# Optimization experiments

Measured on AMD Instinct MI355X. Metric: run time of the kernel, lower is better.

The kernel has to match this reference:

```python
import jax, jax.numpy as jnp
import numpy as np

B, T, F = 64, 512, 512      # batch, timesteps, raw feature dim
D_IN = 1024                 # input_layer units
H = 1024                    # hidden_units
D_OUT = 128                 # output_size


def setup_inputs() -> dict:
    key = jax.random.key(0)
    ks = jax.random.split(key, 10)
    def glorot(k, shape):
        lim = np.sqrt(6.0 / (shape[0] + shape[1])).astype(np.float32)
        return jax.random.uniform(k, shape, jnp.float32, -lim, lim)
    return {
        "x": jax.random.normal(ks[0], (B, T, F), jnp.float32),
        # input Dense (tanh)
        "Wi": glorot(ks[1], (F, D_IN)),
        "bi": jnp.zeros((D_IN,), jnp.float32),
        # LSTM layer 0: kernel, recurrent kernel, bias (init ones, gate order i,f,c,o)
        "W0": glorot(ks[2], (D_IN, 4 * H)),
        "U0": glorot(ks[3], (H, 4 * H)),
        "b0": jnp.ones((4 * H,), jnp.float32),
        # LSTM layer 1
        "W1": glorot(ks[4], (H, 4 * H)),
        "U1": glorot(ks[5], (H, 4 * H)),
        "b1": jnp.ones((4 * H,), jnp.float32),
        # output Dense (tanh)
        "Wo": glorot(ks[6], (H, D_OUT)),
        "bo": jnp.zeros((D_OUT,), jnp.float32),
    }


def _lstm_cell(x, h, c, W, U, b):
    # Keras LSTMCell gate order: i, f, c(candidate), o
    z = x @ W + h @ U + b                      # [B, 4H]
    zi, zf, zc, zo = jnp.split(z, 4, axis=-1)
    i = jax.nn.sigmoid(zi)
    f = jax.nn.sigmoid(zf)
    c_new = f * c + i * jnp.tanh(zc)
    h_new = jax.nn.sigmoid(zo) * jnp.tanh(c_new)
    return h_new, c_new


def reference(x, Wi, bi, W0, U0, b0, W1, U1, b1, Wo, bo):
    b = x.shape[0]
    h = W0.shape[1] // 4
    zeros = jnp.zeros((b, h), x.dtype)
    init = (zeros, zeros, zeros, zeros)  # h0, c0, h1, c1

    def step(carry, xt):
        h0, c0, h1, c1 = carry
        xin = jnp.tanh(xt @ Wi + bi)                    # input Dense
        h0, c0 = _lstm_cell(xin, h0, c0, W0, U0, b0)
        h1, c1 = _lstm_cell(h0, h1, c1, W1, U1, b1)
        return (h0, c0, h1, c1), None

    (h0, c0, h1, c1), _ = jax.lax.scan(step, init, jnp.swapaxes(x, 0, 1))
    return jnp.tanh(h1 @ Wo + bo)  # [B, D_OUT]
```

## Files before the change

### kernel.cpp

```cpp
#include <hip/hip_runtime.h>
#include <math.h>

#define BB 64
#define TT 512
#define FF 512
#define DIN 1024
#define HH 1024
#define G4 4096
#define DOUT 128

typedef _Float16 f16;
typedef _Float16 f16x4 __attribute__((ext_vector_type(4)));
typedef _Float16 f16x8 __attribute__((ext_vector_type(8)));
typedef float f32x4 __attribute__((ext_vector_type(4)));

__device__ __forceinline__ size_t afrag_off(int m, int k) {
    return (size_t)(((k >> 5) * 4 + (m >> 4)) * 512 + (((((k >> 3) & 3) << 4) | (m & 15)) * 8) + (k & 7));
}

__device__ __forceinline__ void store_b128_sc1(void* p, f32x4 v) {
    asm volatile("global_store_dwordx4 %0, %1, off sc1" :: "v"(p), "v"(v) : "memory");
}

__global__ __launch_bounds__(64) void k_pack(
    const float* __restrict__ W, const float* __restrict__ U, f16* __restrict__ out)
{
    const int kstep = blockIdx.x, cg = blockIdx.y, l = threadIdx.x;
    const int n = l & 15, q = l >> 4;
    const int stdcol = (n & 3) * HH + cg * 4 + (n >> 2);
    f16x8 v;
#pragma unroll
    for (int e = 0; e < 8; ++e) {
        int k = kstep * 32 + q * 8 + e;
        float s = (k < DIN) ? W[(size_t)k * G4 + stdcol] : U[(size_t)(k - DIN) * G4 + stdcol];
        v[e] = (f16)s;
    }
    *(f16x8*)(out + ((size_t)(cg * 64 + kstep) * 64 + l) * 8) = v;
}

__global__ __launch_bounds__(64) void k_pack_wi(
    const float* __restrict__ Wi, f16* __restrict__ out)
{
    const int kstep = blockIdx.x;
    const int nt    = blockIdx.y;
    const int l = threadIdx.x;
    const int n = nt * 16 + (l & 15), q = l >> 4;
    f16x8 v;
#pragma unroll
    for (int e = 0; e < 8; ++e)
        v[e] = (f16)Wi[(size_t)(kstep * 32 + q * 8 + e) * DIN + n];
    *(f16x8*)(out + ((size_t)(nt * 16 + kstep) * 64 + l) * 8) = v;
}

__global__ __launch_bounds__(256) void k_dense_in2(
    const float* __restrict__ x, const f16* __restrict__ pWi,
    const float* __restrict__ bi, f16* __restrict__ XinF)
{
    extern __shared__ f16 xs[];
    const int t = blockIdx.x;
    const int tid = threadIdx.x;

#pragma unroll
    for (int it = 0; it < 32; ++it) {
        int idx = tid + it * 256;
        int r = idx >> 7, c4 = idx & 127;
        float4 v = *(const float4*)(x + ((size_t)r * TT + t) * FF + c4 * 4);
        f16x4 hv = {(f16)v.x, (f16)v.y, (f16)v.z, (f16)v.w};
        *(f16x4*)(xs + (size_t)r * 520 + c4 * 4) = hv;
    }
    __syncthreads();

    const int w = tid >> 6, lane = tid & 63;
    const int col = lane & 15, rq = lane >> 4;
#pragma unroll 1
    for (int g = 0; g < 4; ++g) {
        f32x4 acc[4][4];
#pragma unroll
        for (int a = 0; a < 4; ++a)
#pragma unroll
            for (int b = 0; b < 4; ++b) acc[a][b] = (f32x4){0.f, 0.f, 0.f, 0.f};
#pragma unroll 2
        for (int ks2 = 0; ks2 < 16; ++ks2) {
            f16x8 bf[4];
#pragma unroll
            for (int nn = 0; nn < 4; ++nn)
                bf[nn] = *(const f16x8*)(pWi + ((size_t)((w * 16 + g * 4 + nn) * 16 + ks2) * 64 + lane) * 8);
#pragma unroll
            for (int mt = 0; mt < 4; ++mt) {
                f16x8 af = *(const f16x8*)(xs + (size_t)(mt * 16 + col) * 520 + ks2 * 32 + rq * 8);
#pragma unroll
                for (int nn = 0; nn < 4; ++nn)
                    acc[mt][nn] = __builtin_amdgcn_mfma_f32_16x16x32_f16(af, bf[nn], acc[mt][nn], 0, 0, 0);
            }
        }
#pragma unroll
        for (int nn = 0; nn < 4; ++nn) {
            const int j = (w * 16 + g * 4 + nn) * 16 + col;
            const float bb = bi[j];
#pragma unroll
            for (int mt = 0; mt < 4; ++mt)
#pragma unroll
                for (int r = 0; r < 4; ++r)
                    XinF[(size_t)t * (BB * DIN) + afrag_off(mt * 16 + rq * 4 + r, j)]
                        = (f16)tanhf(acc[mt][nn][r] + bb);
        }
    }
}

__global__ __launch_bounds__(512, 2) void k_persist(
    const f16* __restrict__ XinF,
    f16* __restrict__ h0b_, f16* __restrict__ h1b_,
    const f16* __restrict__ pW0, const f16* __restrict__ pW1,
    const float* __restrict__ b0, const float* __restrict__ b1,
    unsigned* __restrict__ flags)
{
    extern __shared__ char smem[];
    f16*   bsh = (f16*)smem;
    float* red = (float*)(smem + 131072);

    const int lay = blockIdx.x & 1;
    const int cgb = blockIdx.x >> 1;
    const int tid = threadIdx.x;
    const int wv = tid >> 6, lane = tid & 63;
    const int kq = wv >> 1, mh = wv & 1;

    unsigned* fl   = flags + (lay ? 1024 : 0);
    unsigned* goO  = flags + 2048 + (lay ? 32 : 0);
    unsigned* go0p = flags + 2048;
    const bool isAgg = (cgb == 0);

    {
        const f16x8* s8 = (const f16x8*)((lay ? pW1 : pW0) + (size_t)(cgb * 2) * 64 * 512);
        f16x8* d8 = (f16x8*)bsh;
#pragma unroll
        for (int it = 0; it < 16; ++it) d8[tid + it * 512] = s8[tid + it * 512];
    }

    const float* bias = lay ? b1 : b0;
    const int erow = tid & 63, ejl = (tid >> 6) & 3;
    const int emt = erow >> 4, esub = erow & 15;
    const int eslq = (esub >> 2) << 4, ereg = esub & 3;
    float bz[2][4];
    float creg[2] = {0.f, 0.f};
    if (tid < 256) {
#pragma unroll
        for (int n = 0; n < 2; ++n) {
            const int jg = (cgb * 2 + n) * 4 + ejl;
#pragma unroll
            for (int g = 0; g < 4; ++g) bz[n][g] = bias[g * HH + jg];
        }
    }

    const size_t HBUF = (size_t)BB * DIN;
    const f16* bq = bsh + (size_t)(kq * 16 * 64 + lane) * 8;
    __syncthreads();

    for (int p = 0; p <= TT; ++p) {
        if (lay == 0 && p == TT) break;
        const bool active = lay ? (p >= 1) : true;

        if (active) {
            const f16* Abase;
            if (lay == 0) Abase = (kq < 2) ? (XinF + (size_t)p * HBUF) : (h0b_ + (size_t)p * HBUF);
            else          Abase = (kq < 2) ? (h0b_ + (size_t)p * HBUF) : (h1b_ + (size_t)(p - 1) * HBUF);
            f16* hw = lay ? (h1b_ + (size_t)p * HBUF) : (h0b_ + (size_t)(p + 1) * HBUF);
            const f16* Ap = Abase + (size_t)(((kq & 1) * 64 + mh * 2) * 512) + (size_t)lane * 8;

            f16x8 a0v[16], a1v[16];
            const bool pre = (lay == 0) && (kq < 2);
            if (pre) {
#pragma unroll
                for (int ii = 0; ii < 16; ++ii) {
                    a0v[ii] = *(const f16x8*)(Ap + (size_t)(ii * 4) * 512);
                    a1v[ii] = *(const f16x8*)(Ap + (size_t)(ii * 4 + 1) * 512);
                }
            }

            if (lay == 0) {
                if (p > 0) {
                    if (tid == 0)
                        while (__hip_atomic_load(go0p, __ATOMIC_RELAXED, __HIP_MEMORY_SCOPE_AGENT) < (unsigned)p)
                            __builtin_amdgcn_s_sleep(1);
                    __syncthreads();
                }
            } else {
                if (tid == 0) {
                    while (__hip_atomic_load(go0p, __ATOMIC_RELAXED, __HIP_MEMORY_SCOPE_AGENT) < (unsigned)p)
                        __builtin_amdgcn_s_sleep(1);
                    while (__hip_atomic_load(goO, __ATOMIC_RELAXED, __HIP_MEMORY_SCOPE_AGENT) < (unsigned)p)
                        __builtin_amdgcn_s_sleep(1);
                }
                __syncthreads();
            }

            if (!pre) {
#pragma unroll
                for (int ii = 0; ii < 16; ++ii) {
                    a0v[ii] = *(const f16x8*)(Ap + (size_t)(ii * 4) * 512);
                    a1v[ii] = *(const f16x8*)(Ap + (size_t)(ii * 4 + 1) * 512);
                }
            }

            f32x4 acc00 = {0.f,0.f,0.f,0.f}, acc01 = {0.f,0.f,0.f,0.f};
            f32x4 acc10 = {0.f,0.f,0.f,0.f}, acc11 = {0.f,0.f,0.f,0.f};
#pragma unroll
            for (int ii = 0; ii < 16; ++ii) {
                f16x8 bb0 = *(const f16x8*)(bq + (size_t)ii * 512);
                f16x8 bb1 = *(const f16x8*)(bq + 32768 + (size_t)ii * 512);
                acc00 = __builtin_amdgcn_mfma_f32_16x16x32_f16(a0v[ii], bb0, acc00, 0, 0, 0);
                acc01 = __builtin_amdgcn_mfma_f32_16x16x32_f16(a0v[ii], bb1, acc01, 0, 0, 0);
                acc10 = __builtin_amdgcn_mfma_f32_16x16x32_f16(a1v[ii], bb0, acc10, 0, 0, 0);
                acc11 = __builtin_amdgcn_mfma_f32_16x16x32_f16(a1v[ii], bb1, acc11, 0, 0, 0);
            }

            f16 hvv[2];
#pragma unroll
            for (int n = 0; n < 2; ++n) {
                f32x4 t0 = n ? acc01 : acc00;
                f32x4 t1 = n ? acc11 : acc10;
                *(f32x4*)(red + (size_t)(kq * 4 + mh * 2)     * 260 + lane * 4) = t0;
                *(f32x4*)(red + (size_t)(kq * 4 + mh * 2 + 1) * 260 + lane * 4) = t1;
                __syncthreads();
                if (tid < 256) {
                    float z[4];
#pragma unroll
                    for (int g = 0; g < 4; ++g) {
                        const int sl = eslq | (ejl * 4 + g);
                        float s = 0.f;
#pragma unroll
                        for (int k2 = 0; k2 < 4; ++k2)
                            s += red[(size_t)(k2 * 4 + emt) * 260 + sl * 4 + ereg];
                        z[g] = s + bz[n][g];
                    }
                    const float ig = 1.f / (1.f + expf(-z[0]));
                    const float fg = 1.f / (1.f + expf(-z[1]));
                    const float cc = tanhf(z[2]);
                    const float og = 1.f / (1.f + expf(-z[3]));
                    const float cn = fg * creg[n] + ig * cc;
                    creg[n] = cn;
                    hvv[n] = (f16)(og * tanhf(cn));
                }
                __syncthreads();
            }

            f16* hrow = (f16*)red;
            if (tid < 256) {
                hrow[erow * 8 + ejl]     = hvv[0];
                hrow[erow * 8 + 4 + ejl] = hvv[1];
            }
            __syncthreads();
            if (tid < 64) {
                f32x4 v = *(f32x4*)(hrow + tid * 8);
                store_b128_sc1(hw + afrag_off(tid, cgb * 8), v);
            }
        }

        asm volatile("s_waitcnt vmcnt(0)" ::: "memory");
        __syncthreads();
        const unsigned tgt = (unsigned)(p + 1);
        if (tid == 0)
            __hip_atomic_store(&fl[cgb], tgt, __ATOMIC_RELAXED, __HIP_MEMORY_SCOPE_AGENT);
        if (isAgg) {
            if (tid < 64) {
                for (;;) {
                    bool ok = (__hip_atomic_load(&fl[lane], __ATOMIC_RELAXED, __HIP_MEMORY_SCOPE_AGENT) >= tgt)
                           && (__hip_atomic_load(&fl[lane + 64], __ATOMIC_RELAXED, __HIP_MEMORY_SCOPE_AGENT) >= tgt);
                    if (__all(ok)) break;
                    __builtin_amdgcn_s_sleep(1);
                }
                if (tid == 0)
                    __hip_atomic_store(goO, tgt, __ATOMIC_RELAXED, __HIP_MEMORY_SCOPE_AGENT);
            }
        }
    }
}

__global__ __launch_bounds__(128) void k_out(
    const f16* __restrict__ h1f, const float* __restrict__ Wo,
    const float* __restrict__ bo, float* __restrict__ out)
{
    __shared__ float hs[HH];
    const int b = blockIdx.x;
    for (int i = threadIdx.x; i < HH; i += 128) hs[i] = (float)h1f[afrag_off(b, i)];
    __syncthreads();
    const int o = threadIdx.x;
    float acc = 0.f;
    for (int k = 0; k < HH; ++k) acc += hs[k] * Wo[k * DOUT + o];
    out[b * DOUT + o] = tanhf(acc + bo[o]);
}

extern "C" void kernel_launch(void* const* d_in, const int* in_sizes, int n_in,
                              void* d_out, int out_size, void* d_ws, size_t ws_size,
                              hipStream_t stream)
{
    const float* x  = (const float*)d_in[0];
    const float* Wi = (const float*)d_in[1];
    const float* bi = (const float*)d_in[2];
    const float* W0 = (const float*)d_in[3];
    const float* U0 = (const float*)d_in[4];
    const float* b0 = (const float*)d_in[5];
    const float* W1 = (const float*)d_in[6];
    const float* U1 = (const float*)d_in[7];
    const float* b1 = (const float*)d_in[8];
    const float* Wo = (const float*)d_in[9];
    const float* bo = (const float*)d_in[10];
    float* out = (float*)d_out;

    f16* ws16 = (f16*)d_ws;
    const size_t HBUF = (size_t)BB * DIN;
    f16* XinF = ws16;
    f16* pW0  = XinF + (size_t)TT * HBUF;
    f16* pW1  = pW0 + (size_t)2048 * G4;
    f16* pWi  = pW1 + (size_t)2048 * G4;
    f16* h0   = pWi + (size_t)FF * DIN;
    f16* h1   = h0 + (size_t)513 * HBUF;
    unsigned* flags = (unsigned*)(h1 + (size_t)513 * HBUF);

    hipMemsetAsync(h0, 0, HBUF * sizeof(f16), stream);
    hipMemsetAsync(h1, 0, HBUF * sizeof(f16), stream);
    hipMemsetAsync(flags, 0, 16384, stream);

    k_pack<<<dim3(64, 256), 64, 0, stream>>>(W0, U0, pW0);
    k_pack<<<dim3(64, 256), 64, 0, stream>>>(W1, U1, pW1);
    k_pack_wi<<<dim3(16, 64), 64, 0, stream>>>(Wi, pWi);

    hipFuncSetAttribute((const void*)k_dense_in2,
                        hipFuncAttributeMaxDynamicSharedMemorySize, 66560);
    k_dense_in2<<<TT, 256, 66560, stream>>>(x, pWi, bi, XinF);

    {
        const int smem_bytes = 131072 + 16640;
        hipFuncSetAttribute((const void*)k_persist,
                            hipFuncAttributeMaxDynamicSharedMemorySize, smem_bytes);
        const f16* XinF_c = XinF;
        const f16* pW0_c = pW0;
        const f16* pW1_c = pW1;
        f16 *h0_v = h0, *h1_v = h1;
        const float *b0_v = b0, *b1_v = b1;
        unsigned* flags_v = flags;
        void* kargs[] = {
            (void*)&XinF_c,
            (void*)&h0_v, (void*)&h1_v,
            (void*)&pW0_c, (void*)&pW1_c,
            (void*)&b0_v, (void*)&b1_v,
            (void*)&flags_v
        };
        hipLaunchCooperativeKernel((void*)k_persist, dim3(256), dim3(512),
                                   kargs, smem_bytes, stream);
    }

    k_out<<<BB, 128, 0, stream>>>(h1 + (size_t)512 * HBUF, Wo, bo, out);
}
```

Measured before the change: 3.392 ms.

## Replace block-wide barrier handshakes with per-wave waits and padded flags

Waves now spin on the go flags themselves, and only waves that actually need a dependency wait: layer-0 waves handling the precomputed input half never wait. The block-wide __syncthreads around the wait is gone. Each flag is padded to its own 64-byte slot to avoid contention. h is written as two 64-bit stores, one per gate-column group, as soon as that group is ready, instead of one 128-bit store after an extra barrier. A-operand loads move inside the MFMA loop, which removes the input prefetch ahead of the wait and drops register pressure. In exchange many more waves now poll global flags concurrently, and only wave 0 drains its stores before publishing the completion flag.

```diff
diff --git a/kernel.cpp b/kernel.cpp
--- a/kernel.cpp
+++ b/kernel.cpp
@@ -12,14 +12,20 @@
 typedef _Float16 f16;
 typedef _Float16 f16x4 __attribute__((ext_vector_type(4)));
 typedef _Float16 f16x8 __attribute__((ext_vector_type(8)));
+typedef float f32x2 __attribute__((ext_vector_type(2)));
 typedef float f32x4 __attribute__((ext_vector_type(4)));
 
 __device__ __forceinline__ size_t afrag_off(int m, int k) {
     return (size_t)(((k >> 5) * 4 + (m >> 4)) * 512 + (((((k >> 3) & 3) << 4) | (m & 15)) * 8) + (k & 7));
 }
 
-__device__ __forceinline__ void store_b128_sc1(void* p, f32x4 v) {
-    asm volatile("global_store_dwordx4 %0, %1, off sc1" :: "v"(p), "v"(v) : "memory");
+__device__ __forceinline__ void store_b64_sc1(void* p, f32x2 v) {
+    asm volatile("global_store_dwordx2 %0, %1, off sc1" :: "v"(p), "v"(v) : "memory");
+}
+
+__device__ __forceinline__ void wave_wait(const unsigned* w, unsigned tgt) {
+    while (__hip_atomic_load(w, __ATOMIC_RELAXED, __HIP_MEMORY_SCOPE_AGENT) < tgt)
+        __builtin_amdgcn_s_sleep(1);
 }
 
 __global__ __launch_bounds__(64) void k_pack(
@@ -115,8 +121,9 @@
     unsigned* __restrict__ flags)
 {
     extern __shared__ char smem[];
-    f16*   bsh = (f16*)smem;
-    float* red = (float*)(smem + 131072);
+    f16*   bsh  = (f16*)smem;
+    float* red  = (float*)(smem + 131072);
+    f16*   hrow = (f16*)(smem + 131072 + 16640);
 
     const int lay = blockIdx.x & 1;
     const int cgb = blockIdx.x >> 1;
@@ -124,10 +131,10 @@
     const int wv = tid >> 6, lane = tid & 63;
     const int kq = wv >> 1, mh = wv & 1;
 
-    unsigned* fl   = flags + (lay ? 1024 : 0);
-    unsigned* goO  = flags + 2048 + (lay ? 32 : 0);
-    unsigned* go0p = flags + 2048;
-    const bool isAgg = (cgb == 0);
+    unsigned* fl  = flags + (lay ? 2048 : 0);
+    unsigned* go0 = flags + 4096;
+    unsigned* go1 = flags + 4096 + 16;
+    unsigned* goMine = lay ? go1 : go0;
 
     {
         const f16x8* s8 = (const f16x8*)((lay ? pW1 : pW0) + (size_t)(cgb * 2) * 64 * 512);
@@ -160,60 +167,40 @@
         const bool active = lay ? (p >= 1) : true;
 
         if (active) {
-            const f16* Abase;
-            if (lay == 0) Abase = (kq < 2) ? (XinF + (size_t)p * HBUF) : (h0b_ + (size_t)p * HBUF);
-            else          Abase = (kq < 2) ? (h0b_ + (size_t)p * HBUF) : (h1b_ + (size_t)(p - 1) * HBUF);
-            f16* hw = lay ? (h1b_ + (size_t)p * HBUF) : (h0b_ + (size_t)(p + 1) * HBUF);
-            const f16* Ap = Abase + (size_t)(((kq & 1) * 64 + mh * 2) * 512) + (size_t)lane * 8;
-
-            f16x8 a0v[16], a1v[16];
-            const bool pre = (lay == 0) && (kq < 2);
-            if (pre) {
-#pragma unroll
-                for (int ii = 0; ii < 16; ++ii) {
-                    a0v[ii] = *(const f16x8*)(Ap + (size_t)(ii * 4) * 512);
-                    a1v[ii] = *(const f16x8*)(Ap + (size_t)(ii * 4 + 1) * 512);
-                }
-            }
-
+            const f16 *A1, *A2;
+            f16* hw;
             if (lay == 0) {
-                if (p > 0) {
-                    if (tid == 0)
-                        while (__hip_atomic_load(go0p, __ATOMIC_RELAXED, __HIP_MEMORY_SCOPE_AGENT) < (unsigned)p)
-                            __builtin_amdgcn_s_sleep(1);
-                    __syncthreads();
-                }
+                A1 = XinF + (size_t)p * HBUF;
+                A2 = h0b_ + (size_t)p * HBUF;
+                hw = h0b_ + (size_t)(p + 1) * HBUF;
             } else {
-                if (tid == 0) {
-                    while (__hip_atomic_load(go0p, __ATOMIC_RELAXED, __HIP_MEMORY_SCOPE_AGENT) < (unsigned)p)
-                        __builtin_amdgcn_s_sleep(1);
-                    while (__hip_atomic_load(goO, __ATOMIC_RELAXED, __HIP_MEMORY_SCOPE_AGENT) < (unsigned)p)
-                        __builtin_amdgcn_s_sleep(1);
-                }
-                __syncthreads();
-            }
-
-            if (!pre) {
-#pragma unroll
-                for (int ii = 0; ii < 16; ++ii) {
-                    a0v[ii] = *(const f16x8*)(Ap + (size_t)(ii * 4) * 512);
-                    a1v[ii] = *(const f16x8*)(Ap + (size_t)(ii * 4 + 1) * 512);
-                }
+                A1 = h0b_ + (size_t)p * HBUF;
+                A2 = h1b_ + (size_t)(p - 1) * HBUF;
+                hw = h1b_ + (size_t)p * HBUF;
+            }
+            const f16* Ap = ((kq < 2) ? A1 : A2)
+                          + (size_t)(((kq & 1) * 64 + mh * 2) * 512) + (size_t)lane * 8;
+
+            if (lay == 0) {
+                if (kq >= 2 && p > 0) wave_wait(go0, (unsigned)p);
+            } else {
+                wave_wait(kq < 2 ? go0 : go1, (unsigned)p);
             }
 
             f32x4 acc00 = {0.f,0.f,0.f,0.f}, acc01 = {0.f,0.f,0.f,0.f};
             f32x4 acc10 = {0.f,0.f,0.f,0.f}, acc11 = {0.f,0.f,0.f,0.f};
 #pragma unroll
             for (int ii = 0; ii < 16; ++ii) {
+                f16x8 a0  = *(const f16x8*)(Ap + (size_t)(ii * 4) * 512);
+                f16x8 a1  = *(const f16x8*)(Ap + (size_t)(ii * 4 + 1) * 512);
                 f16x8 bb0 = *(const f16x8*)(bq + (size_t)ii * 512);
                 f16x8 bb1 = *(const f16x8*)(bq + 32768 + (size_t)ii * 512);
-                acc00 = __builtin_amdgcn_mfma_f32_16x16x32_f16(a0v[ii], bb0, acc00, 0, 0, 0);
-                acc01 = __builtin_amdgcn_mfma_f32_16x16x32_f16(a0v[ii], bb1, acc01, 0, 0, 0);
-                acc10 = __builtin_amdgcn_mfma_f32_16x16x32_f16(a1v[ii], bb0, acc10, 0, 0, 0);
-                acc11 = __builtin_amdgcn_mfma_f32_16x16x32_f16(a1v[ii], bb1, acc11, 0, 0, 0);
-            }
-
-            f16 hvv[2];
+                acc00 = __builtin_amdgcn_mfma_f32_16x16x32_f16(a0, bb0, acc00, 0, 0, 0);
+                acc01 = __builtin_amdgcn_mfma_f32_16x16x32_f16(a0, bb1, acc01, 0, 0, 0);
+                acc10 = __builtin_amdgcn_mfma_f32_16x16x32_f16(a1, bb0, acc10, 0, 0, 0);
+                acc11 = __builtin_amdgcn_mfma_f32_16x16x32_f16(a1, bb1, acc11, 0, 0, 0);
+            }
+
 #pragma unroll
             for (int n = 0; n < 2; ++n) {
                 f32x4 t0 = n ? acc01 : acc00;
@@ -238,39 +225,35 @@
                     const float og = 1.f / (1.f + expf(-z[3]));
                     const float cn = fg * creg[n] + ig * cc;
                     creg[n] = cn;
-                    hvv[n] = (f16)(og * tanhf(cn));
+                    hrow[n * 256 + erow * 4 + ejl] = (f16)(og * tanhf(cn));
                 }
                 __syncthreads();
-            }
-
-            f16* hrow = (f16*)red;
-            if (tid < 256) {
-                hrow[erow * 8 + ejl]     = hvv[0];
-                hrow[erow * 8 + 4 + ejl] = hvv[1];
-            }
-            __syncthreads();
-            if (tid < 64) {
-                f32x4 v = *(f32x4*)(hrow + tid * 8);
-                store_b128_sc1(hw + afrag_off(tid, cgb * 8), v);
-            }
-        }
-
-        asm volatile("s_waitcnt vmcnt(0)" ::: "memory");
-        __syncthreads();
+                if (tid < 64) {
+                    f32x2 v = *(f32x2*)(hrow + n * 256 + tid * 4);
+                    store_b64_sc1(hw + afrag_off(tid, cgb * 8 + n * 4), v);
+                }
+            }
+        }
+
         const unsigned tgt = (unsigned)(p + 1);
-        if (tid == 0)
-            __hip_atomic_store(&fl[cgb], tgt, __ATOMIC_RELAXED, __HIP_MEMORY_SCOPE_AGENT);
-        if (isAgg) {
-            if (tid < 64) {
-                for (;;) {
-                    bool ok = (__hip_atomic_load(&fl[lane], __ATOMIC_RELAXED, __HIP_MEMORY_SCOPE_AGENT) >= tgt)
-                           && (__hip_atomic_load(&fl[lane + 64], __ATOMIC_RELAXED, __HIP_MEMORY_SCOPE_AGENT) >= tgt);
-                    if (__all(ok)) break;
-                    __builtin_amdgcn_s_sleep(1);
-                }
-                if (tid == 0)
-                    __hip_atomic_store(goO, tgt, __ATOMIC_RELAXED, __HIP_MEMORY_SCOPE_AGENT);
-            }
+        if (tid < 64) {
+            if (active) asm volatile("s_waitcnt vmcnt(0)" ::: "memory");
+            if (tid == 0)
+                __hip_atomic_store(&fl[cgb * 16], tgt, __ATOMIC_RELAXED,
+                                   __HIP_MEMORY_SCOPE_AGENT);
+        }
+        if (cgb == 0 && tid < 64) {
+            for (;;) {
+                bool ok = (__hip_atomic_load(&fl[lane * 16], __ATOMIC_RELAXED,
+                                             __HIP_MEMORY_SCOPE_AGENT) >= tgt)
+                       && (__hip_atomic_load(&fl[(lane + 64) * 16], __ATOMIC_RELAXED,
+                                             __HIP_MEMORY_SCOPE_AGENT) >= tgt);
+                if (__all(ok)) break;
+                __builtin_amdgcn_s_sleep(1);
+            }
+            if (tid == 0)
+                __hip_atomic_store(goMine, tgt, __ATOMIC_RELAXED,
+                                   __HIP_MEMORY_SCOPE_AGENT);
         }
     }
 }
@@ -318,7 +301,7 @@
 
     hipMemsetAsync(h0, 0, HBUF * sizeof(f16), stream);
     hipMemsetAsync(h1, 0, HBUF * sizeof(f16), stream);
-    hipMemsetAsync(flags, 0, 16384, stream);
+    hipMemsetAsync(flags, 0, 32768, stream);
 
     k_pack<<<dim3(64, 256), 64, 0, stream>>>(W0, U0, pW0);
     k_pack<<<dim3(64, 256), 64, 0, stream>>>(W1, U1, pW1);
@@ -329,7 +312,7 @@
     k_dense_in2<<<TT, 256, 66560, stream>>>(x, pWi, bi, XinF);
 
     {
-        const int smem_bytes = 131072 + 16640;
+        const int smem_bytes = 131072 + 16640 + 1024;
         hipFuncSetAttribute((const void*)k_persist,
                             hipFuncAttributeMaxDynamicSharedMemorySize, smem_bytes);
         const f16* XinF_c = XinF;
```

Result: slower. 4.350 ms (+28.3%).
